# Optimization experiments

Measured on AMD Instinct MI355X. Metric: run time of the kernel, lower is better.

## Reference

```python
import jax, jax.numpy as jnp
import numpy as np

B, S, E = 4, 2048, 1024
H, Dh = 16, 64


def setup_inputs() -> dict:
    key = jax.random.key(0)
    ks = jax.random.split(key, 9)
    scale_in = 1.0 / np.sqrt(E)
    scale_out = 1.0 / np.sqrt(H * Dh)
    x = jax.random.normal(ks[0], (B, S, E), dtype=jnp.float32)
    # Per-head projection weights stacked over heads: [H, E, Dh]
    Wq = jax.random.uniform(ks[1], (H, E, Dh), jnp.float32, -scale_in, scale_in)
    bq = jax.random.uniform(ks[2], (H, Dh), jnp.float32, -scale_in, scale_in)
    Wk = jax.random.uniform(ks[3], (H, E, Dh), jnp.float32, -scale_in, scale_in)
    bk = jax.random.uniform(ks[4], (H, Dh), jnp.float32, -scale_in, scale_in)
    Wv = jax.random.uniform(ks[5], (H, E, Dh), jnp.float32, -scale_in, scale_in)
    bv = jax.random.uniform(ks[6], (H, Dh), jnp.float32, -scale_in, scale_in)
    # Output projection: [H*Dh, E]
    Wo = jax.random.uniform(ks[7], (H * Dh, E), jnp.float32, -scale_out, scale_out)
    bo = jax.random.uniform(ks[8], (E,), jnp.float32, -scale_out, scale_out)
    return {"x": x, "Wq": Wq, "bq": bq, "Wk": Wk, "bk": bk,
            "Wv": Wv, "bv": bv, "Wo": Wo, "bo": bo}


def reference(x, Wq, bq, Wk, bk, Wv, bv, Wo, bo):
    # Per-head linear projections, batched over heads: [B, H, S, Dh]
    q = jnp.einsum('bse,hed->bhsd', x, Wq) + bq[None, :, None, :]
    k = jnp.einsum('bse,hed->bhsd', x, Wk) + bk[None, :, None, :]
    v = jnp.einsum('bse,hed->bhsd', x, Wv) + bv[None, :, None, :]
    scale = 1.0 / jnp.sqrt(jnp.asarray(Dh, dtype=x.dtype))
    scores = jnp.einsum('bhsd,bhtd->bhst', q, k) * scale  # [B, H, S, S]
    weights = jax.nn.softmax(scores, axis=-1)
    z = jnp.einsum('bhst,bhtd->bhsd', weights, v)  # [B, H, S, Dh]
    # Concat heads in module order: [B, S, H*Dh]
    z = jnp.transpose(z, (0, 2, 1, 3)).reshape(B, S, H * Dh)
    return z @ Wo + bo
```

## Files before the change

### kernel.cpp

```cpp
#include <hip/hip_runtime.h>
#include <hip/hip_bf16.h>

#define B_  4
#define S_  2048
#define E_  1024
#define H_  16
#define DH_ 64
#define M_  (B_*S_)
#define HD_ (H_*DH_)

typedef unsigned short u16;
typedef __attribute__((ext_vector_type(8))) __bf16 bf16x8;
typedef __attribute__((ext_vector_type(4))) __bf16 bf16x4;
typedef __attribute__((ext_vector_type(4))) float  f32x4;

#if __has_builtin(__builtin_amdgcn_exp2f)
#define EXP2F __builtin_amdgcn_exp2f
#else
#define EXP2F __builtin_exp2f
#endif

#define QSCALE 0.18033688011112042f

__device__ __forceinline__ void g2l16(const void* g, void* l) {
  __builtin_amdgcn_global_load_lds(
      (const __attribute__((address_space(1))) void*)g,
      (__attribute__((address_space(3))) void*)l, 16, 0, 0);
}

__device__ __forceinline__ u16 f2bf(float f) {
  union { float f; unsigned u; } v; v.f = f;
  unsigned r = v.u + 0x7FFFu + ((v.u >> 16) & 1u);
  return (u16)(r >> 16);
}

__global__ __launch_bounds__(256) void cvt_x_kernel(const float* __restrict__ x,
                                                    u16* __restrict__ xb) {
  int i = blockIdx.x * 256 + threadIdx.x;
  float4 v = ((const float4*)x)[i];
  ushort4 o;
  o.x = f2bf(v.x); o.y = f2bf(v.y); o.z = f2bf(v.z); o.w = f2bf(v.w);
  ((ushort4*)xb)[i] = o;
}

__global__ __launch_bounds__(256) void pack_wqkv_kernel(
    const float* __restrict__ Wq, const float* __restrict__ Wk,
    const float* __restrict__ Wv, u16* __restrict__ wt) {
  __shared__ u16 tile[64][66];
  int p = blockIdx.z, h = blockIdx.y, e0 = blockIdx.x * 64;
  const float* src = (p == 0 ? Wq : (p == 1 ? Wk : Wv)) + h * (E_ * DH_);
  int tid = threadIdx.x;
#pragma unroll
  for (int r = 0; r < 16; ++r) {
    int idx = r * 256 + tid;
    int el = idx >> 6, d = idx & 63;
    tile[el][d] = f2bf(src[(e0 + el) * DH_ + d]);
  }
  __syncthreads();
  u16* dst = wt + (p * HD_ + h * DH_) * E_;
#pragma unroll
  for (int r = 0; r < 16; ++r) {
    int idx = r * 256 + tid;
    int d = idx >> 6, el = idx & 63;
    dst[d * E_ + e0 + el] = tile[el][d];
  }
}

__global__ __launch_bounds__(256) void pack_wo_kernel(const float* __restrict__ Wo,
                                                      u16* __restrict__ wt) {
  __shared__ u16 tile[64][66];
  int c0 = blockIdx.y * 64, e0 = blockIdx.x * 64;
  int tid = threadIdx.x;
#pragma unroll
  for (int r = 0; r < 16; ++r) {
    int idx = r * 256 + tid;
    int cl = idx >> 6, el = idx & 63;
    tile[cl][el] = f2bf(Wo[(c0 + cl) * E_ + e0 + el]);
  }
  __syncthreads();
#pragma unroll
  for (int r = 0; r < 16; ++r) {
    int idx = r * 256 + tid;
    int er = idx >> 6, cl = idx & 63;
    wt[(e0 + er) * HD_ + c0 + cl] = tile[cl][er];
  }
}

__global__ __launch_bounds__(256) void pack_bias_kernel(
    const float* __restrict__ bq, const float* __restrict__ bk,
    const float* __restrict__ bv, float* __restrict__ bb) {
  int i = blockIdx.x * 256 + threadIdx.x;
  const float* s = (i < 1024 ? bq : (i < 2048 ? bk : bv));
  bb[i] = s[i & 1023];
}

__global__ __launch_bounds__(256) void transpose_v_kernel(
    const u16* __restrict__ vin, u16* __restrict__ vout) {
  __shared__ u16 t[64][72];
  const int tid = threadIdx.x;
  const int bh = blockIdx.y, st = blockIdx.x * 64;
  const u16* src = vin + ((size_t)((bh >> 4) * S_ + st)) * HD_ + (bh & 15) * 64;
#pragma unroll
  for (int rr = 0; rr < 2; ++rr) {
    int idx = rr * 256 + tid;
    int s = idx >> 3, ch = idx & 7;
    *(uint4*)&t[s][ch * 8] = *(const uint4*)(src + s * HD_ + ch * 8);
  }
  __syncthreads();
  u16* dst = vout + ((size_t)bh) * DH_ * S_ + st;
#pragma unroll
  for (int rr = 0; rr < 2; ++rr) {
    int idx = rr * 256 + tid;
    int d = idx >> 3, sc = (idx & 7) * 8;
    ushort4 o0, o1;
    o0.x = t[sc + 0][d]; o0.y = t[sc + 1][d]; o0.z = t[sc + 2][d]; o0.w = t[sc + 3][d];
    o1.x = t[sc + 4][d]; o1.y = t[sc + 5][d]; o1.z = t[sc + 6][d]; o1.w = t[sc + 7][d];
    *(ushort4*)(dst + (size_t)d * S_ + sc) = o0;
    *(ushort4*)(dst + (size_t)d * S_ + sc + 4) = o1;
  }
}

template <int MODE>
__global__ __launch_bounds__(256) void gemm_bt_kernel(
    const u16* __restrict__ A, const u16* __restrict__ Bt,
    const float* __restrict__ bias,
    u16* __restrict__ oQ, u16* __restrict__ oK, u16* __restrict__ oV,
    float* __restrict__ oF) {
  constexpr int K = 1024;
  __shared__ __align__(16) u16 As[128 * 32];
  __shared__ __align__(16) u16 Bs[128 * 32];
  const int tid = threadIdx.x;
  const int lane = tid & 63, wv = tid >> 6;
  const int wm = (wv >> 1) * 64, wn = (wv & 1) * 64;
  const int q4 = lane >> 4, lm = lane & 15;
  const int tileM = blockIdx.y * 128, tileN = blockIdx.x * 128;

  const int c0 = tid, c1 = tid + 256;
  const u16* gA0 = A + (tileM + (c0 >> 2)) * K + (((c0 & 3) ^ ((c0 >> 2) & 3)) * 8);
  const u16* gA1 = A + (tileM + (c1 >> 2)) * K + (((c1 & 3) ^ ((c1 >> 2) & 3)) * 8);
  const u16* gB0 = Bt + (tileN + (c0 >> 2)) * K + (((c0 & 3) ^ ((c0 >> 2) & 3)) * 8);
  const u16* gB1 = Bt + (tileN + (c1 >> 2)) * K + (((c1 & 3) ^ ((c1 >> 2) & 3)) * 8);
  u16* lA0 = As + c0 * 8; u16* lA1 = As + c1 * 8;
  u16* lB0 = Bs + c0 * 8; u16* lB1 = Bs + c1 * 8;

  f32x4 acc[4][4] = {};

  int aoff[4], boff[4];
#pragma unroll
  for (int i = 0; i < 4; ++i) {
    int ra = wm + i * 16 + lm;
    aoff[i] = ra * 32 + ((q4 ^ (ra & 3)) * 8);
    int rb = wn + i * 16 + lm;
    boff[i] = rb * 32 + ((q4 ^ (rb & 3)) * 8);
  }

  for (int k0 = 0; k0 < K; k0 += 32) {
    g2l16(gA0 + k0, lA0);
    g2l16(gA1 + k0, lA1);
    g2l16(gB0 + k0, lB0);
    g2l16(gB1 + k0, lB1);
    __syncthreads();
    bf16x8 af[4], bf[4];
#pragma unroll
    for (int i = 0; i < 4; ++i) af[i] = *(const bf16x8*)(As + aoff[i]);
#pragma unroll
    for (int j = 0; j < 4; ++j) bf[j] = *(const bf16x8*)(Bs + boff[j]);
#pragma unroll
    for (int i = 0; i < 4; ++i)
#pragma unroll
      for (int j = 0; j < 4; ++j)
        acc[i][j] = __builtin_amdgcn_mfma_f32_16x16x32_bf16(af[i], bf[j], acc[i][j], 0, 0, 0);
    __syncthreads();
  }

#pragma unroll
  for (int j = 0; j < 4; ++j) {
    int n = tileN + wn + j * 16 + lm;
    float bs = bias[n];
#pragma unroll
    for (int i = 0; i < 4; ++i) {
#pragma unroll
      for (int r = 0; r < 4; ++r) {
        int m = tileM + wm + i * 16 + q4 * 4 + r;
        float val = acc[i][j][r] + bs;
        if (MODE == 1) {
          oF[m * HD_ + n] = val;
        } else {
          int proj = n >> 10, cc = n & 1023;
          u16* optr = (proj == 0 ? oQ : (proj == 1 ? oK : oV));
          float scl = (proj == 0 ? QSCALE : 1.0f);
          optr[m * 1024 + cc] = f2bf(val * scl);
        }
      }
    }
  }
}

__global__ __launch_bounds__(256, 2) void flash_kernel(
    const u16* __restrict__ Q, const u16* __restrict__ Kb,
    const u16* __restrict__ Vt, u16* __restrict__ Z) {
  __shared__ __align__(16) u16 Ks[2][64 * 64];
  __shared__ __align__(16) u16 Vs[2][64 * 64];
  __shared__ __align__(16) u16 Ps[4][64 * 64];
  const int tid = threadIdx.x, lane = tid & 63, wv = tid >> 6;
  const int q4 = lane >> 4, lm = lane & 15;

  const int bid = blockIdx.x;
  const int bh = bid >> 3, qt = bid & 7;
  const int b = bh >> 4, h = bh & 15;

  const u16* qbase = Q + ((size_t)(b * S_ + qt * 256)) * HD_ + h * DH_;
  const u16* kbase = Kb + (size_t)b * S_ * HD_ + h * DH_;
  const u16* vbase = Vt + ((size_t)(b * H_ + h)) * DH_ * S_;
  u16* zbase = Z + ((size_t)(b * S_ + qt * 256)) * HD_ + h * DH_;

  const int c0 = tid,       r0 = c0 >> 3, s0 = ((c0 & 7) ^ (r0 & 7)) * 8;
  const int c1 = tid + 256, r1 = c1 >> 3, s1 = ((c1 & 7) ^ (r1 & 7)) * 8;

  bf16x8 qf[4][2];
#pragma unroll
  for (int qs = 0; qs < 4; ++qs)
#pragma unroll
    for (int dc = 0; dc < 2; ++dc)
      qf[qs][dc] = *(const bf16x8*)(qbase + (wv * 64 + qs * 16 + lm) * HD_ + dc * 32 + q4 * 8);

  const bf16x8 ones = {(__bf16)1.f, (__bf16)1.f, (__bf16)1.f, (__bf16)1.f,
                       (__bf16)1.f, (__bf16)1.f, (__bf16)1.f, (__bf16)1.f};

  int koff[4][2], voff[2][4], pwoff[4], proff[2];
#pragma unroll
  for (int kb = 0; kb < 4; ++kb)
#pragma unroll
    for (int dc = 0; dc < 2; ++dc) {
      int row = kb * 16 + lm;
      koff[kb][dc] = row * 64 + (((dc * 4 + q4) ^ (row & 7)) * 8);
    }
#pragma unroll
  for (int ck = 0; ck < 2; ++ck)
#pragma unroll
    for (int db = 0; db < 4; ++db) {
      int row = db * 16 + lm;
      voff[ck][db] = row * 64 + (((ck * 4 + q4) ^ (row & 7)) * 8);
    }
#pragma unroll
  for (int kb = 0; kb < 4; ++kb) {
    int kc = kb * 2 + (q4 >> 1);
    pwoff[kb] = lm * 64 + ((kc ^ (lm & 7)) * 8) + (q4 & 1) * 4;
  }
#pragma unroll
  for (int ck = 0; ck < 2; ++ck)
    proff[ck] = lm * 64 + (((ck * 4 + q4) ^ (lm & 7)) * 8);

  f32x4 oacc[4][4] = {};
  f32x4 liacc[4] = {};
  u16* Pw = Ps[wv];

  {
    g2l16(kbase + r0 * HD_ + s0, Ks[0] + c0 * 8);
    g2l16(kbase + r1 * HD_ + s1, Ks[0] + c1 * 8);
    g2l16(vbase + r0 * S_ + s0, Vs[0] + c0 * 8);
    g2l16(vbase + r1 * S_ + s1, Vs[0] + c1 * 8);
  }

  for (int t = 0; t < 32; ++t) {
    const int pb = t & 1;
    __syncthreads();
    if (t < 31) {
      const u16* kt = kbase + (size_t)(t + 1) * 64 * HD_;
      const u16* vt = vbase + (t + 1) * 64;
      g2l16(kt + r0 * HD_ + s0, Ks[1 - pb] + c0 * 8);
      g2l16(kt + r1 * HD_ + s1, Ks[1 - pb] + c1 * 8);
      g2l16(vt + r0 * S_ + s0, Vs[1 - pb] + c0 * 8);
      g2l16(vt + r1 * S_ + s1, Vs[1 - pb] + c1 * 8);
    }
    const u16* Kp = Ks[pb];
    const u16* Vp = Vs[pb];

#pragma unroll
    for (int kb = 0; kb < 4; ++kb) {
      bf16x8 k0 = *(const bf16x8*)(Kp + koff[kb][0]);
      bf16x8 k1 = *(const bf16x8*)(Kp + koff[kb][1]);
#pragma unroll
      for (int qs = 0; qs < 4; ++qs) {
        f32x4 sc = {};
        sc = __builtin_amdgcn_mfma_f32_16x16x32_bf16(k0, qf[qs][0], sc, 0, 0, 0);
        sc = __builtin_amdgcn_mfma_f32_16x16x32_bf16(k1, qf[qs][1], sc, 0, 0, 0);
        f32x4 p;
#pragma unroll
        for (int r = 0; r < 4; ++r) p[r] = EXP2F(sc[r]);
        bf16x4 pbv = __builtin_convertvector(p, bf16x4);
        *(bf16x4*)(Pw + qs * (16 * 64) + pwoff[kb]) = pbv;
      }
    }
    asm volatile("s_waitcnt lgkmcnt(0)" ::: "memory");

#pragma unroll
    for (int ck = 0; ck < 2; ++ck) {
      bf16x8 pf[4];
#pragma unroll
      for (int qs = 0; qs < 4; ++qs)
        pf[qs] = *(const bf16x8*)(Pw + qs * (16 * 64) + proff[ck]);
#pragma unroll
      for (int qs = 0; qs < 4; ++qs)
        liacc[qs] = __builtin_amdgcn_mfma_f32_16x16x32_bf16(pf[qs], ones, liacc[qs], 0, 0, 0);
#pragma unroll
      for (int db = 0; db < 4; ++db) {
        bf16x8 vf = *(const bf16x8*)(Vp + voff[ck][db]);
#pragma unroll
        for (int qs = 0; qs < 4; ++qs)
          oacc[qs][db] = __builtin_amdgcn_mfma_f32_16x16x32_bf16(pf[qs], vf, oacc[qs][db], 0, 0, 0);
      }
    }
  }

#pragma unroll
  for (int qs = 0; qs < 4; ++qs) {
    float rin[4];
#pragma unroll
    for (int r = 0; r < 4; ++r) rin[r] = 1.f / liacc[qs][r];
#pragma unroll
    for (int db = 0; db < 4; ++db)
#pragma unroll
      for (int r = 0; r < 4; ++r)
        zbase[(wv * 64 + qs * 16 + q4 * 4 + r) * HD_ + db * 16 + lm] =
            f2bf(oacc[qs][db][r] * rin[r]);
  }
}

extern "C" void kernel_launch(void* const* d_in, const int* in_sizes, int n_in,
                              void* d_out, int out_size, void* d_ws, size_t ws_size,
                              hipStream_t stream) {
  const float* x  = (const float*)d_in[0];
  const float* Wq = (const float*)d_in[1];
  const float* bq = (const float*)d_in[2];
  const float* Wk = (const float*)d_in[3];
  const float* bk = (const float*)d_in[4];
  const float* Wv = (const float*)d_in[5];
  const float* bv = (const float*)d_in[6];
  const float* Wo = (const float*)d_in[7];
  const float* bo = (const float*)d_in[8];
  float* out = (float*)d_out;

  char* w = (char*)d_ws;
  u16*   xb    = (u16*)w;   w += (size_t)M_ * E_ * 2;
  u16*   wqkvT = (u16*)w;   w += (size_t)3 * HD_ * E_ * 2;
  u16*   woT   = (u16*)w;   w += (size_t)E_ * HD_ * 2;
  float* bqkv  = (float*)w; w += (size_t)3 * HD_ * 4;
  u16*   qB    = (u16*)w;   w += (size_t)M_ * HD_ * 2;
  u16*   kB    = (u16*)w;   w += (size_t)M_ * HD_ * 2;
  u16*   vT    = (u16*)w;   w += (size_t)M_ * HD_ * 2;
  u16*   zB    = (u16*)w;   w += (size_t)M_ * HD_ * 2;
  u16*   vB    = zB;

  cvt_x_kernel<<<dim3(M_ * E_ / 4 / 256), 256, 0, stream>>>(x, xb);
  pack_wqkv_kernel<<<dim3(16, 16, 3), 256, 0, stream>>>(Wq, Wk, Wv, wqkvT);
  pack_wo_kernel<<<dim3(16, 16), 256, 0, stream>>>(Wo, woT);
  pack_bias_kernel<<<dim3(12), 256, 0, stream>>>(bq, bk, bv, bqkv);
  gemm_bt_kernel<0><<<dim3(24, 64), 256, 0, stream>>>(xb, wqkvT, bqkv, qB, kB, vB, nullptr);
  transpose_v_kernel<<<dim3(32, 64), 256, 0, stream>>>(vB, vT);
  flash_kernel<<<dim3(512), 256, 0, stream>>>(qB, kB, vT, zB);
  gemm_bt_kernel<1><<<dim3(8, 64), 256, 0, stream>>>(zB, woT, bo, nullptr, nullptr, nullptr, out);
}
```

Before: 290.5 us.

## Keep softmax probabilities in registers via permuted K rows; drop bias pack kernel

The flash kernel no longer writes P to shared memory and reads it back. K rows are loaded into LDS in a permuted order so that each lane's MFMA score outputs line up directly with the A-operand layout needed for the PV MFMA, and the fragments are joined with a shuffle. This removes the Ps buffer (64KB of LDS) and its waitcnt, which allows raising launch bounds to 3 blocks per CU. Separately, the bias pack kernel is removed and the QKV GEMM selects among bq, bk and bv directly, saving one launch. The cost is higher register pressure from holding pfr, and correctness depends on the row permutation being exact.

After: 441.3 us. 51.9% more time.

```diff
diff --git a/kernel.cpp b/kernel.cpp
--- a/kernel.cpp
+++ b/kernel.cpp
@@ -84,14 +84,6 @@
     int er = idx >> 6, cl = idx & 63;
     wt[(e0 + er) * HD_ + c0 + cl] = tile[cl][er];
   }
-}
-
-__global__ __launch_bounds__(256) void pack_bias_kernel(
-    const float* __restrict__ bq, const float* __restrict__ bk,
-    const float* __restrict__ bv, float* __restrict__ bb) {
-  int i = blockIdx.x * 256 + threadIdx.x;
-  const float* s = (i < 1024 ? bq : (i < 2048 ? bk : bv));
-  bb[i] = s[i & 1023];
 }
 
 __global__ __launch_bounds__(256) void transpose_v_kernel(
@@ -123,7 +115,8 @@
 template <int MODE>
 __global__ __launch_bounds__(256) void gemm_bt_kernel(
     const u16* __restrict__ A, const u16* __restrict__ Bt,
-    const float* __restrict__ bias,
+    const float* __restrict__ b0, const float* __restrict__ b1,
+    const float* __restrict__ b2,
     u16* __restrict__ oQ, u16* __restrict__ oK, u16* __restrict__ oV,
     float* __restrict__ oF) {
   constexpr int K = 1024;
@@ -176,7 +169,15 @@
 #pragma unroll
   for (int j = 0; j < 4; ++j) {
     int n = tileN + wn + j * 16 + lm;
-    float bs = bias[n];
+    float bs;
+    int proj = 0, cc = n;
+    if (MODE == 1) {
+      bs = b0[n];
+    } else {
+      proj = n >> 10; cc = n & 1023;
+      const float* bp = (proj == 0 ? b0 : (proj == 1 ? b1 : b2));
+      bs = bp[cc];
+    }
 #pragma unroll
     for (int i = 0; i < 4; ++i) {
 #pragma unroll
@@ -186,7 +187,6 @@
         if (MODE == 1) {
           oF[m * HD_ + n] = val;
         } else {
-          int proj = n >> 10, cc = n & 1023;
           u16* optr = (proj == 0 ? oQ : (proj == 1 ? oK : oV));
           float scl = (proj == 0 ? QSCALE : 1.0f);
           optr[m * 1024 + cc] = f2bf(val * scl);
@@ -196,12 +196,11 @@
   }
 }
 
-__global__ __launch_bounds__(256, 2) void flash_kernel(
+__global__ __launch_bounds__(256, 3) void flash_kernel(
     const u16* __restrict__ Q, const u16* __restrict__ Kb,
     const u16* __restrict__ Vt, u16* __restrict__ Z) {
   __shared__ __align__(16) u16 Ks[2][64 * 64];
   __shared__ __align__(16) u16 Vs[2][64 * 64];
-  __shared__ __align__(16) u16 Ps[4][64 * 64];
   const int tid = threadIdx.x, lane = tid & 63, wv = tid >> 6;
   const int q4 = lane >> 4, lm = lane & 15;
 
@@ -216,6 +215,8 @@
 
   const int c0 = tid,       r0 = c0 >> 3, s0 = ((c0 & 7) ^ (r0 & 7)) * 8;
   const int c1 = tid + 256, r1 = c1 >> 3, s1 = ((c1 & 7) ^ (r1 & 7)) * 8;
+  const int kr0 = ((r0 >> 4) & 1) * 32 + ((r0 >> 2) & 3) * 8 + (r0 >> 5) * 4 + (r0 & 3);
+  const int kr1 = ((r1 >> 4) & 1) * 32 + ((r1 >> 2) & 3) * 8 + (r1 >> 5) * 4 + (r1 & 3);
 
   bf16x8 qf[4][2];
 #pragma unroll
@@ -227,7 +228,7 @@
   const bf16x8 ones = {(__bf16)1.f, (__bf16)1.f, (__bf16)1.f, (__bf16)1.f,
                        (__bf16)1.f, (__bf16)1.f, (__bf16)1.f, (__bf16)1.f};
 
-  int koff[4][2], voff[2][4], pwoff[4], proff[2];
+  int koff[4][2], voff[2][4];
 #pragma unroll
   for (int kb = 0; kb < 4; ++kb)
 #pragma unroll
@@ -242,22 +243,13 @@
       int row = db * 16 + lm;
       voff[ck][db] = row * 64 + (((ck * 4 + q4) ^ (row & 7)) * 8);
     }
-#pragma unroll
-  for (int kb = 0; kb < 4; ++kb) {
-    int kc = kb * 2 + (q4 >> 1);
-    pwoff[kb] = lm * 64 + ((kc ^ (lm & 7)) * 8) + (q4 & 1) * 4;
-  }
-#pragma unroll
-  for (int ck = 0; ck < 2; ++ck)
-    proff[ck] = lm * 64 + (((ck * 4 + q4) ^ (lm & 7)) * 8);
 
   f32x4 oacc[4][4] = {};
   f32x4 liacc[4] = {};
-  u16* Pw = Ps[wv];
 
   {
-    g2l16(kbase + r0 * HD_ + s0, Ks[0] + c0 * 8);
-    g2l16(kbase + r1 * HD_ + s1, Ks[0] + c1 * 8);
+    g2l16(kbase + kr0 * HD_ + s0, Ks[0] + c0 * 8);
+    g2l16(kbase + kr1 * HD_ + s1, Ks[0] + c1 * 8);
     g2l16(vbase + r0 * S_ + s0, Vs[0] + c0 * 8);
     g2l16(vbase + r1 * S_ + s1, Vs[0] + c1 * 8);
   }
@@ -268,14 +260,15 @@
     if (t < 31) {
       const u16* kt = kbase + (size_t)(t + 1) * 64 * HD_;
       const u16* vt = vbase + (t + 1) * 64;
-      g2l16(kt + r0 * HD_ + s0, Ks[1 - pb] + c0 * 8);
-      g2l16(kt + r1 * HD_ + s1, Ks[1 - pb] + c1 * 8);
+      g2l16(kt + kr0 * HD_ + s0, Ks[1 - pb] + c0 * 8);
+      g2l16(kt + kr1 * HD_ + s1, Ks[1 - pb] + c1 * 8);
       g2l16(vt + r0 * S_ + s0, Vs[1 - pb] + c0 * 8);
       g2l16(vt + r1 * S_ + s1, Vs[1 - pb] + c1 * 8);
     }
     const u16* Kp = Ks[pb];
     const u16* Vp = Vs[pb];
 
+    bf16x4 pfr[4][4];
 #pragma unroll
     for (int kb = 0; kb < 4; ++kb) {
       bf16x8 k0 = *(const bf16x8*)(Kp + koff[kb][0]);
@@ -288,18 +281,17 @@
         f32x4 p;
 #pragma unroll
         for (int r = 0; r < 4; ++r) p[r] = EXP2F(sc[r]);
-        bf16x4 pbv = __builtin_convertvector(p, bf16x4);
-        *(bf16x4*)(Pw + qs * (16 * 64) + pwoff[kb]) = pbv;
+        pfr[qs][kb] = __builtin_convertvector(p, bf16x4);
       }
     }
-    asm volatile("s_waitcnt lgkmcnt(0)" ::: "memory");
 
 #pragma unroll
     for (int ck = 0; ck < 2; ++ck) {
       bf16x8 pf[4];
 #pragma unroll
       for (int qs = 0; qs < 4; ++qs)
-        pf[qs] = *(const bf16x8*)(Pw + qs * (16 * 64) + proff[ck]);
+        pf[qs] = __builtin_shufflevector(pfr[qs][ck], pfr[qs][ck + 2],
+                                         0, 1, 2, 3, 4, 5, 6, 7);
 #pragma unroll
       for (int qs = 0; qs < 4; ++qs)
         liacc[qs] = __builtin_amdgcn_mfma_f32_16x16x32_bf16(pf[qs], ones, liacc[qs], 0, 0, 0);
@@ -345,7 +337,6 @@
   u16*   xb    = (u16*)w;   w += (size_t)M_ * E_ * 2;
   u16*   wqkvT = (u16*)w;   w += (size_t)3 * HD_ * E_ * 2;
   u16*   woT   = (u16*)w;   w += (size_t)E_ * HD_ * 2;
-  float* bqkv  = (float*)w; w += (size_t)3 * HD_ * 4;
   u16*   qB    = (u16*)w;   w += (size_t)M_ * HD_ * 2;
   u16*   kB    = (u16*)w;   w += (size_t)M_ * HD_ * 2;
   u16*   vT    = (u16*)w;   w += (size_t)M_ * HD_ * 2;
@@ -355,9 +346,10 @@
   cvt_x_kernel<<<dim3(M_ * E_ / 4 / 256), 256, 0, stream>>>(x, xb);
   pack_wqkv_kernel<<<dim3(16, 16, 3), 256, 0, stream>>>(Wq, Wk, Wv, wqkvT);
   pack_wo_kernel<<<dim3(16, 16), 256, 0, stream>>>(Wo, woT);
-  pack_bias_kernel<<<dim3(12), 256, 0, stream>>>(bq, bk, bv, bqkv);
-  gemm_bt_kernel<0><<<dim3(24, 64), 256, 0, stream>>>(xb, wqkvT, bqkv, qB, kB, vB, nullptr);
+  gemm_bt_kernel<0><<<dim3(24, 64), 256, 0, stream>>>(xb, wqkvT, bq, bk, bv,
+                                                      qB, kB, vB, nullptr);
   transpose_v_kernel<<<dim3(32, 64), 256, 0, stream>>>(vB, vT);
   flash_kernel<<<dim3(512), 256, 0, stream>>>(qB, kB, vT, zB);
-  gemm_bt_kernel<1><<<dim3(8, 64), 256, 0, stream>>>(zB, woT, bo, nullptr, nullptr, nullptr, out);
-}
+  gemm_bt_kernel<1><<<dim3(8, 64), 256, 0, stream>>>(zB, woT, bo, nullptr, nullptr,
+                                                     nullptr, nullptr, nullptr, out);
+}
```
